# Kernel tuning notes

Measured on AMD Instinct MI355X. Metric: run time of the kernel, lower is better.

Reference implementation:

```python
import jax, jax.numpy as jnp
import numpy as np

APERTURE = 128
LN_EPS = 1e-6

def _layer_norm(y, g, b):
    mu = jnp.mean(y, axis=-1, keepdims=True)
    var = jnp.var(y, axis=-1, keepdims=True)
    return (y - mu) / jnp.sqrt(var + LN_EPS) * g + b

def setup_inputs() -> dict:
    key = jax.random.key(0)
    ks = jax.random.split(key, 12)
    B, S, D = 4, 4096, 1024
    gain = np.sqrt(2.0)
    xav = lambda k, fan_out, fan_in: jax.random.uniform(
        k, (fan_out, fan_in), jnp.float32,
        -gain * np.sqrt(6.0 / (fan_in + fan_out)), gain * np.sqrt(6.0 / (fan_in + fan_out)))
    return {
        "x": jax.random.normal(ks[0], (B, S, D), jnp.float32),
        "Wq": xav(ks[1], D, D),
        "Wk": xav(ks[2], D, D),
        "Wv": xav(ks[3], D, D),
        "Wo": xav(ks[4], D, D),
        "k1_w": xav(ks[5], D, D),
        "k1_b": jnp.full((D,), 0.1, jnp.float32),
        "k2_w": xav(ks[6], 1, D),
        "k2_b": jnp.full((1,), 0.1, jnp.float32),
        "ln_g": jnp.ones((D,), jnp.float32),
        "ln_b": jnp.zeros((D,), jnp.float32),
    }

def reference(x, Wq, Wk, Wv, Wo, k1_w, k1_b, k2_w, k2_b, ln_g, ln_b):
    B, S, D = x.shape
    scale = jnp.float32(1.0 / np.sqrt(D))
    neg_inf = jnp.float32(-np.inf)

    Q = x @ Wq.T  # [B,S,D]
    K = x @ Wk.T
    V = x @ Wv.T

    e = jnp.einsum('bsd,btd->bst', Q, K) * scale  # [B,S,S]

    # ignore_self: -inf on the diagonal
    i = jnp.arange(S)[:, None]
    j = jnp.arange(S)[None, :]
    e = jnp.where(i == j, neg_inf, e)

    # banded aperture mask: tril(e, ap) * triu(e, -ap); zeros of the product -> -inf
    d = j - i
    scope = jnp.where(d <= APERTURE, e, 0.0) * jnp.where(d >= -APERTURE, e, 0.0)
    e = jnp.where(scope == 0.0, neg_inf, e)

    alpha = jax.nn.softmax(e, axis=2)
    c = jnp.einsum('bst,btd->bsd', alpha, V)
    c = c @ Wo.T

    y = c + x
    y = _layer_norm(y, ln_g, ln_b)
    y = jax.nn.relu(y @ k1_w.T + k1_b)
    y = _layer_norm(y, ln_g, ln_b)
    y = jax.nn.sigmoid(y @ k2_w.T + k2_b)  # [B,S,1]
    return y.reshape(B, S)
```

## Files before the change

kernel.cpp:

```cpp
#include <hip/hip_runtime.h>
#include <math.h>

#define DD 1024
#define SS 4096
#define AP 128
#define LN_EPS 1e-6f
#define BK 32
#define BAND 384

typedef __bf16 bf16;
typedef __attribute__((ext_vector_type(4))) __bf16 bf16x4;
typedef __attribute__((ext_vector_type(8))) __bf16 bf16x8;
typedef __attribute__((ext_vector_type(4))) float f32x4;

#define GLOAD_LDS16(g, l)                                                   \
    __builtin_amdgcn_global_load_lds(                                        \
        (const __attribute__((address_space(1))) void*)(g),                  \
        (__attribute__((address_space(3))) void*)(l), 16, 0, 0)

__global__ __launch_bounds__(256) void prep_all(const float* __restrict__ x,
                                                const float* __restrict__ Wq,
                                                const float* __restrict__ Wk,
                                                const float* __restrict__ Wv,
                                                const float* __restrict__ Wo,
                                                const float* __restrict__ k1w,
                                                const float* __restrict__ k1b,
                                                const float* __restrict__ lng,
                                                const float* __restrict__ lnb,
                                                bf16* __restrict__ xb,
                                                bf16* __restrict__ Wob,
                                                bf16* __restrict__ k1g,
                                                bf16* __restrict__ Wtb,
                                                float* __restrict__ u1,
                                                float* __restrict__ c1b) {
    __shared__ float tile[64][65];
    const int bid = blockIdx.x;
    const int tid = threadIdx.x;
    if (bid < 16384) {
        const int i = (bid * 256 + tid) * 4;
        const float4 a = *(const float4*)(x + i);
        bf16x4 o;
        o[0] = (__bf16)a.x; o[1] = (__bf16)a.y; o[2] = (__bf16)a.z; o[3] = (__bf16)a.w;
        *(bf16x4*)(xb + i) = o;
        return;
    }
    if (bid < 18432) {
        const int b2 = bid - 16384;
        const int sel = b2 >> 10;
        const int bb = b2 & 1023;
        const float* s = sel ? k1w : Wo;
        bf16* d = sel ? k1g : Wob;
        const int i = (bb * 256 + tid) * 4;
        float4 a = *(const float4*)(s + i);
        if (sel) {
            const float4 g4 = *(const float4*)(lng + (i & (DD - 1)));
            a.x *= g4.x; a.y *= g4.y; a.z *= g4.z; a.w *= g4.w;
        }
        bf16x4 o;
        o[0] = (__bf16)a.x; o[1] = (__bf16)a.y; o[2] = (__bf16)a.z; o[3] = (__bf16)a.w;
        *(bf16x4*)(d + i) = o;
        return;
    }
    if (bid < 19200) {
        const int t = bid - 18432;
        const int tz = t >> 8;
        const int tb_ = t & 255;
        const float* in = (tz == 0) ? Wq : (tz == 1) ? Wk : Wv;
        bf16* out = Wtb + ((size_t)tz << 20);
        const int r0 = (tb_ >> 4) * 64, c0 = (tb_ & 15) * 64;
        const int lr = tid >> 4;
        const int lc = (tid & 15) * 4;
#pragma unroll
        for (int rr = 0; rr < 4; rr++) {
            const int row = lr + rr * 16;
            const float4 v = *(const float4*)(in + (size_t)(r0 + row) * DD + c0 + lc);
            tile[row][lc] = v.x; tile[row][lc + 1] = v.y;
            tile[row][lc + 2] = v.z; tile[row][lc + 3] = v.w;
        }
        __syncthreads();
#pragma unroll
        for (int rr = 0; rr < 4; rr++) {
            const int row = lr + rr * 16;
            bf16x4 o;
            o[0] = (__bf16)tile[lc + 0][row];
            o[1] = (__bf16)tile[lc + 1][row];
            o[2] = (__bf16)tile[lc + 2][row];
            o[3] = (__bf16)tile[lc + 3][row];
            *(bf16x4*)(out + (size_t)(c0 + row) * DD + r0 + lc) = o;
        }
        return;
    }
    const int pv = bid - 19200;
    const int lane = tid & 63, wave = tid >> 6;
    const int n = pv * 4 + wave;
    const float* row = k1w + (size_t)n * DD + lane * 16;
    float su = 0.f, sb = 0.f;
#pragma unroll
    for (int q = 0; q < 4; q++) {
        const float4 a = *(const float4*)(row + q * 4);
        const float4 g4 = *(const float4*)(lng + lane * 16 + q * 4);
        const float4 b4 = *(const float4*)(lnb + lane * 16 + q * 4);
        su += a.x * g4.x + a.y * g4.y + a.z * g4.z + a.w * g4.w;
        sb += a.x * b4.x + a.y * b4.y + a.z * b4.z + a.w * b4.w;
    }
#pragma unroll
    for (int off = 32; off > 0; off >>= 1) {
        su += __shfl_xor(su, off);
        sb += __shfl_xor(sb, off);
    }
    if (lane == 0) {
        u1[n] = su;
        c1b[n] = sb + k1b[n];
    }
}

__global__ __launch_bounds__(256) void gemm_pair(const bf16* __restrict__ A0,
                                                 const bf16* __restrict__ W0,
                                                 bf16* __restrict__ O0,
                                                 const bf16* __restrict__ A1,
                                                 const bf16* __restrict__ W1,
                                                 bf16* __restrict__ O1) {
    const bf16* A = blockIdx.z ? A1 : A0;
    const bf16* W = blockIdx.z ? W1 : W0;
    bf16* O = blockIdx.z ? O1 : O0;
    __shared__ bf16 As[128 * BK];
    __shared__ bf16 Bs[128 * BK];
    const int tid = threadIdx.x;
    const int lane = tid & 63;
    const int wave = tid >> 6;
    const int wm = wave & 1;
    const int wn = wave >> 1;
    const int m0 = blockIdx.y * 128;
    const int n0 = blockIdx.x * 128;

    const int c = wave * 64 + lane;
    const int ar = c >> 2;
    const int ac = (c & 3) << 3;
    char* AsB = (char*)As;
    char* BsB = (char*)Bs;
    const int lr = lane & 15;
    const int lk = (lane >> 4) << 3;

    f32x4 acc[4][4] = {};

    for (int kt = 0; kt < DD; kt += BK) {
        const bf16* ga0 = A + (size_t)(m0 + ar) * DD + kt + ac;
        const bf16* gb0 = W + (size_t)(n0 + ar) * DD + kt + ac;
        GLOAD_LDS16(ga0, AsB + wave * 1024);
        GLOAD_LDS16(ga0 + (size_t)64 * DD, AsB + 4096 + wave * 1024);
        GLOAD_LDS16(gb0, BsB + wave * 1024);
        GLOAD_LDS16(gb0 + (size_t)64 * DD, BsB + 4096 + wave * 1024);
        __syncthreads();

        bf16x8 af[4], bfr[4];
#pragma unroll
        for (int i = 0; i < 4; i++)
            af[i] = *(const bf16x8*)&As[(wm * 64 + i * 16 + lr) * BK + lk];
#pragma unroll
        for (int j = 0; j < 4; j++)
            bfr[j] = *(const bf16x8*)&Bs[(wn * 64 + j * 16 + lr) * BK + lk];
#pragma unroll
        for (int i = 0; i < 4; i++)
#pragma unroll
            for (int j = 0; j < 4; j++)
                acc[i][j] = __builtin_amdgcn_mfma_f32_16x16x32_bf16(af[i], bfr[j], acc[i][j], 0, 0, 0);
        __syncthreads();
    }

#pragma unroll
    for (int i = 0; i < 4; i++) {
        const int row = m0 + wm * 64 + i * 16 + ((lane >> 4) << 2);
#pragma unroll
        for (int j = 0; j < 4; j++) {
            const int col = n0 + wn * 64 + j * 16 + (lane & 15);
#pragma unroll
            for (int rr = 0; rr < 4; rr++)
                O[(size_t)(row + rr) * DD + col] = (__bf16)acc[i][j][rr];
        }
    }
}


#define KL_STAGE_A(tt, hh, bb)                                               \
    {                                                                        \
        const bf16* gp_ = Aop + gofsA + (tt) * 64 + (hh) * 32;               \
        GLOAD_LDS16(gp_, smem + (bb) + (hh) * 16384 + ldsW);                 \
        GLOAD_LDS16(gp_ + (size_t)128 * DD,                                  \
                    smem + (bb) + (hh) * 16384 + 8192 + ldsW);               \
    }
#define KL_STAGE_B(tt, hh, bb)                                               \
    {                                                                        \
        const bf16* gp_ = Bop + gofsB + (tt) * 64 + (hh) * 32;               \
        GLOAD_LDS16(gp_, smem + (bb) + 32768 + (hh) * 16384 + ldsW);         \
        GLOAD_LDS16(gp_ + (size_t)128 * DD,                                  \
                    smem + (bb) + 32768 + (hh) * 16384 + 8192 + ldsW);       \
    }
#define KL_READS_A(ks, mh)                                                   \
    af[0] = *(const bf16x8*)(sA + bufo + (ks) * 16384 + (mh) * 4096);        \
    af[1] = *(const bf16x8*)(sA + bufo + (ks) * 16384 + (mh) * 4096 + 1024); \
    af[2] = *(const bf16x8*)(sA + bufo + (ks) * 16384 + (mh) * 4096 + 2048); \
    af[3] = *(const bf16x8*)(sA + bufo + (ks) * 16384 + (mh) * 4096 + 3072);
#define KL_READS_B(ks)                                                       \
    bfr[0] = *(const bf16x8*)(sB + bufo + (ks) * 16384);                     \
    bfr[1] = *(const bf16x8*)(sB + bufo + (ks) * 16384 + 1024);              \
    bfr[2] = *(const bf16x8*)(sB + bufo + (ks) * 16384 + 2048);              \
    bfr[3] = *(const bf16x8*)(sB + bufo + (ks) * 16384 + 3072);
#define KL_MFMA4(I, MH)                                                      \
    acc[(MH) * 4 + I][0] = __builtin_amdgcn_mfma_f32_16x16x32_bf16(af[I], bfr[0], acc[(MH) * 4 + I][0], 0, 0, 0); \
    acc[(MH) * 4 + I][1] = __builtin_amdgcn_mfma_f32_16x16x32_bf16(af[I], bfr[1], acc[(MH) * 4 + I][1], 0, 0, 0); \
    acc[(MH) * 4 + I][2] = __builtin_amdgcn_mfma_f32_16x16x32_bf16(af[I], bfr[2], acc[(MH) * 4 + I][2], 0, 0, 0); \
    acc[(MH) * 4 + I][3] = __builtin_amdgcn_mfma_f32_16x16x32_bf16(af[I], bfr[3], acc[(MH) * 4 + I][3], 0, 0, 0);
#define KL_MFMA16(MH)                                                        \
    __builtin_amdgcn_s_setprio(1);                                           \
    KL_MFMA4(0, MH) KL_MFMA4(1, MH) KL_MFMA4(2, MH) KL_MFMA4(3, MH)          \
    __builtin_amdgcn_s_setprio(0);
#define KL_BARRIER(N) asm volatile("s_waitcnt vmcnt(" #N ")\n\ts_barrier" ::: "memory")

__device__ __forceinline__ void kloop256(const bf16* __restrict__ Aop,
                                         const bf16* __restrict__ Bop,
                                         const int m0, const int n0,
                                         char* smem, f32x4 (&acc)[8][4],
                                         const int tid, const int lane,
                                         const int wave, const int wm, const int wn) {
    const int grow = tid >> 2;
    const int gslot = (tid & 3) ^ ((tid >> 3) & 3);
    const size_t gofsA = (size_t)(m0 + grow) * DD + gslot * 8;
    const size_t gofsB = (size_t)(n0 + grow) * DD + gslot * 8;
    const int ldsW = wave * 1024;
    const int sxo = (((lane >> 4) ^ ((lane >> 1) & 3)) << 4);
    const char* sA = smem + wm * 8192 + (lane & 15) * 64 + sxo;
    const char* sB = smem + 32768 + wn * 4096 + (lane & 15) * 64 + sxo;

    bf16x8 af[4], bfr[4];

    KL_STAGE_A(0, 0, 0) KL_STAGE_B(0, 0, 0)
    KL_STAGE_A(0, 1, 0) KL_STAGE_B(0, 1, 0)
    KL_STAGE_A(1, 0, 65536) KL_STAGE_B(1, 0, 65536)

    int bufo = 0;
    for (int t = 0; t < 15; t++) {
        const int nb = bufo ^ 65536;
        KL_BARRIER(8);
        KL_READS_A(0, 0) KL_READS_B(0)
        KL_STAGE_A(t + 1, 1, nb)
        KL_MFMA16(0)
        KL_READS_A(0, 1)
        KL_STAGE_B(t + 1, 1, nb)
        KL_MFMA16(1)
        KL_BARRIER(8);
        KL_READS_A(1, 0) KL_READS_B(1)
        if (t < 14) { KL_STAGE_A(t + 2, 0, bufo) }
        KL_MFMA16(0)
        KL_READS_A(1, 1)
        if (t < 14) { KL_STAGE_B(t + 2, 0, bufo) }
        KL_MFMA16(1)
        bufo = nb;
    }
    KL_BARRIER(4);
    KL_READS_A(0, 0) KL_READS_B(0)
    KL_MFMA16(0)
    KL_READS_A(0, 1)
    KL_MFMA16(1)
    KL_BARRIER(0);
    KL_READS_A(1, 0) KL_READS_B(1)
    KL_MFMA16(0)
    KL_READS_A(1, 1)
    KL_MFMA16(1)
}

__global__ __launch_bounds__(512) void gemm_uv(const bf16* __restrict__ xb,
                                               const bf16* __restrict__ Gt,
                                               const bf16* __restrict__ W2,
                                               bf16* __restrict__ Ub,
                                               bf16* __restrict__ Vt2) {
    __shared__ char smem[131072];
    const int s = blockIdx.x;
    const int half = s >> 8;
    const int sh = s & 255;
    const int p = (sh & 7) | ((sh >> 5) << 3);
    const int q = (sh >> 3) & 3;
    const bf16* A;
    const bf16* W;
    bf16* O;
    int m0, n0;
    size_t ldo;
    if (half == 0) {
        A = xb; W = Gt; O = Ub;
        m0 = p * 256; n0 = q * 256; ldo = DD;
    } else {
        A = W2; W = xb; O = Vt2;
        m0 = q * 256; n0 = p * 256; ldo = (size_t)4 * SS;
    }
    const int tid = threadIdx.x;
    const int lane = tid & 63;
    const int wave = tid >> 6;
    const int wm = wave & 1;
    const int wn = wave >> 1;

    f32x4 acc[8][4] = {};
    kloop256(A, W, m0, n0, smem, acc, tid, lane, wave, wm, wn);

#pragma unroll
    for (int a = 0; a < 8; a++) {
        const int row = m0 + wm * 128 + a * 16 + ((lane >> 4) << 2);
#pragma unroll
        for (int j = 0; j < 4; j++) {
            const int col = n0 + wn * 64 + j * 16 + (lane & 15);
#pragma unroll
            for (int rr = 0; rr < 4; rr++)
                O[(size_t)(row + rr) * ldo + col] = (__bf16)acc[a][j][rr];
        }
    }
}

__global__ __launch_bounds__(512) void gemm_k1(const bf16* __restrict__ T,
                                               const bf16* __restrict__ k1g,
                                               const float* __restrict__ part_t,
                                               const float* __restrict__ u1,
                                               const float* __restrict__ c1b,
                                               const float* __restrict__ lng,
                                               const float* __restrict__ k2w,
                                               float* __restrict__ part_h) {
    __shared__ char smem[131072];
    __shared__ float lmu[256], lrs[256];
    const int m0 = blockIdx.x * 256;
    const int n0 = blockIdx.y * 256;
    const int tid = threadIdx.x;
    const int lane = tid & 63;
    const int wave = tid >> 6;
    const int wm = wave & 1;
    const int wn = wave >> 1;

    if (tid < 256) {
        const float* p = part_t + (size_t)(m0 + tid) * 32;
        float s1 = 0.f, s2 = 0.f;
#pragma unroll
        for (int s = 0; s < 8; s++) {
            const float4 v = *(const float4*)(p + s * 4);
            s1 += v.x + v.z;
            s2 += v.y + v.w;
        }
        const float m = s1 * (1.f / DD);
        lmu[tid] = m;
        lrs[tid] = rsqrtf(s2 * (1.f / DD) - m * m + LN_EPS);
    }
    __syncthreads();

    f32x4 acc[8][4] = {};
    kloop256(T, k1g, m0, n0, smem, acc, tid, lane, wave, wm, wn);

    float u1v[4], cbv[4], ugv[4];
#pragma unroll
    for (int j = 0; j < 4; j++) {
        const int col = n0 + wn * 64 + j * 16 + (lane & 15);
        u1v[j] = u1[col];
        cbv[j] = c1b[col];
        ugv[j] = lng[col] * k2w[col];
    }
    const int strip = blockIdx.y * 4 + wn;
#pragma unroll
    for (int a = 0; a < 8; a++) {
#pragma unroll
        for (int rr = 0; rr < 4; rr++) {
            const int lrow = wm * 128 + a * 16 + ((lane >> 4) << 2) + rr;
            const int row = m0 + lrow;
            const float mr = lmu[lrow], rs = lrs[lrow];
            float s1 = 0.f, s2 = 0.f, s3 = 0.f;
#pragma unroll
            for (int j = 0; j < 4; j++) {
                const float v = rs * (acc[a][j][rr] - mr * u1v[j]) + cbv[j];
                const float h = fmaxf(v, 0.f);
                s1 += h; s2 += h * h; s3 += h * ugv[j];
            }
#pragma unroll
            for (int off = 8; off > 0; off >>= 1) {
                s1 += __shfl_xor(s1, off);
                s2 += __shfl_xor(s2, off);
                s3 += __shfl_xor(s3, off);
            }
            if ((lane & 15) == 0) {
                float* p = part_h + (size_t)row * 48 + strip * 3;
                p[0] = s1; p[1] = s2; p[2] = s3;
            }
        }
    }
}

__global__ __launch_bounds__(512) void attn_sp(const bf16* __restrict__ U,
                                               const bf16* __restrict__ X,
                                               bf16* __restrict__ P) {
    __shared__ bf16 As[64 * BK];
    __shared__ bf16 Bs[384 * BK];
    const int s = blockIdx.x;
    const int t = (s & 7) * 32 + ((s >> 3) >> 1) * 2 + ((s >> 3) & 1);
    const int tid = threadIdx.x;
    const int lane = tid & 63;
    const int wave = tid >> 6;
    const int wm = wave & 1;
    const int wn = wave >> 1;
    const int m0 = t * 64;
    const long w0 = (long)(t >> 1) * 128 - 128;

    const int grow = tid >> 2;
    const int gslot = (tid & 3) ^ ((tid >> 3) & 3);
    const size_t gofsA = (size_t)(m0 + (grow & 63)) * DD + gslot * 8;
    const long gofsB = (w0 + grow) * (long)DD + gslot * 8;
    const int ldsW = wave * 1024;
    const int sxo = (((lane >> 4) ^ ((lane >> 1) & 3)) << 4);
    const char* sA = (const char*)As + (lane & 15) * 64 + sxo;
    const char* sB = (const char*)Bs + (lane & 15) * 64 + sxo;

    f32x4 acc[2][6] = {};

    for (int kt = 0; kt < DD; kt += BK) {
        if (wave < 4) { GLOAD_LDS16(U + gofsA + kt, (char*)As + ldsW); }
        GLOAD_LDS16(X + gofsB + kt, (char*)Bs + ldsW);
        GLOAD_LDS16(X + gofsB + (long)128 * DD + kt, (char*)Bs + 8192 + ldsW);
        GLOAD_LDS16(X + gofsB + (long)256 * DD + kt, (char*)Bs + 16384 + ldsW);
        __syncthreads();

        bf16x8 af[2], bfr[6];
#pragma unroll
        for (int i = 0; i < 2; i++)
            af[i] = *(const bf16x8*)(sA + wm * 2048 + i * 1024);
#pragma unroll
        for (int j = 0; j < 6; j++)
            bfr[j] = *(const bf16x8*)(sB + wn * 6144 + j * 1024);
#pragma unroll
        for (int i = 0; i < 2; i++)
#pragma unroll
            for (int j = 0; j < 6; j++)
                acc[i][j] = __builtin_amdgcn_mfma_f32_16x16x32_bf16(af[i], bfr[j], acc[i][j], 0, 0, 0);
        __syncthreads();
    }

    float* lredm = (float*)As;
    float* lreds = lredm + 256;
    const int rbase = wm * 32 + ((lane >> 4) << 2);
    const int ib = (t << 6) & (SS - 1);
    const int jst = ((t >> 1) & 31) * 128 - 128;
    const float scale = 0.03125f;

    float pmx[2][4];
#pragma unroll
    for (int i = 0; i < 2; i++)
#pragma unroll
        for (int rr = 0; rr < 4; rr++) {
            const int irow = ib + rbase + i * 16 + rr;
            float mx = -INFINITY;
#pragma unroll
            for (int j = 0; j < 6; j++) {
                const int jg = jst + wn * 96 + j * 16 + (lane & 15);
                const int dj = jg - irow;
                const bool valid = (jg >= 0) && (jg < SS) && (dj != 0) && (dj <= AP) && (dj >= -AP);
                const float sv = valid ? acc[i][j][rr] * scale : -INFINITY;
                acc[i][j][rr] = sv;
                mx = fmaxf(mx, sv);
            }
#pragma unroll
            for (int off = 8; off > 0; off >>= 1) mx = fmaxf(mx, __shfl_xor(mx, off));
            pmx[i][rr] = mx;
        }
    if ((lane & 15) == 0) {
#pragma unroll
        for (int i = 0; i < 2; i++)
#pragma unroll
            for (int rr = 0; rr < 4; rr++)
                lredm[(rbase + i * 16 + rr) * 4 + wn] = pmx[i][rr];
    }
    __syncthreads();

    float lsum[2][4], mv[2][4];
#pragma unroll
    for (int i = 0; i < 2; i++)
#pragma unroll
        for (int rr = 0; rr < 4; rr++) {
            const int ri = (rbase + i * 16 + rr) * 4;
            mv[i][rr] = fmaxf(fmaxf(lredm[ri], lredm[ri + 1]),
                              fmaxf(lredm[ri + 2], lredm[ri + 3]));
            float su = 0.f;
#pragma unroll
            for (int j = 0; j < 6; j++) {
                const float e = __expf(acc[i][j][rr] - mv[i][rr]);
                acc[i][j][rr] = e;
                su += e;
            }
#pragma unroll
            for (int off = 8; off > 0; off >>= 1) su += __shfl_xor(su, off);
            lsum[i][rr] = su;
        }
    if ((lane & 15) == 0) {
#pragma unroll
        for (int i = 0; i < 2; i++)
#pragma unroll
            for (int rr = 0; rr < 4; rr++)
                lreds[(rbase + i * 16 + rr) * 4 + wn] = lsum[i][rr];
    }
    __syncthreads();

#pragma unroll
    for (int i = 0; i < 2; i++)
#pragma unroll
        for (int rr = 0; rr < 4; rr++) {
            const int ri = (rbase + i * 16 + rr) * 4;
            const float inv = 1.f / (lreds[ri] + lreds[ri + 1] + lreds[ri + 2] + lreds[ri + 3]);
            const size_t ro = (size_t)(m0 + rbase + i * 16 + rr) * BAND;
#pragma unroll
            for (int j = 0; j < 6; j++)
                P[ro + wn * 96 + j * 16 + (lane & 15)] = (__bf16)(acc[i][j][rr] * inv);
        }
}

__global__ __launch_bounds__(512) void attn_pv_mfma(const bf16* __restrict__ P,
                                                    const bf16* __restrict__ Vt,
                                                    const bf16* __restrict__ xres,
                                                    bf16* __restrict__ T,
                                                    float* __restrict__ part_t) {
    __shared__ bf16 As[128 * BK];
    __shared__ bf16 Bs[256 * BK];
    const int tid = threadIdx.x;
    const int lane = tid & 63;
    const int wave = tid >> 6;
    const int wm = wave & 1;
    const int wn = wave >> 1;
    const int t = blockIdx.x;
    const int m0 = t * 128;
    const int n0 = blockIdx.y * 256;
    const bf16* Wb = Vt + (long)t * 128 - 128;

    const int ar = tid >> 2;
    const int ac = (tid & 3) << 3;
    char* AsB = (char*)As;
    char* BsB = (char*)Bs;
    const int lr = lane & 15;
    const int lk = (lane >> 4) << 3;

    f32x4 acc[4][4] = {};

    for (int kt = 0; kt < BAND; kt += BK) {
        const bf16* ga0 = P + (size_t)(m0 + ar) * BAND + kt + ac;
        const bf16* gb0 = Wb + (size_t)(n0 + ar) * (4 * SS) + kt + ac;
        GLOAD_LDS16(ga0, AsB + wave * 1024);
        GLOAD_LDS16(gb0, BsB + wave * 1024);
        GLOAD_LDS16(gb0 + (size_t)128 * (4 * SS), BsB + 8192 + wave * 1024);
        __syncthreads();

        bf16x8 af[4], bfr[4];
#pragma unroll
        for (int i = 0; i < 4; i++)
            af[i] = *(const bf16x8*)&As[(wm * 64 + i * 16 + lr) * BK + lk];
#pragma unroll
        for (int j = 0; j < 4; j++)
            bfr[j] = *(const bf16x8*)&Bs[(wn * 64 + j * 16 + lr) * BK + lk];
#pragma unroll
        for (int i = 0; i < 4; i++)
#pragma unroll
            for (int j = 0; j < 4; j++)
                acc[i][j] = __builtin_amdgcn_mfma_f32_16x16x32_bf16(af[i], bfr[j], acc[i][j], 0, 0, 0);
        __syncthreads();
    }

    const int strip = blockIdx.y * 4 + wn;
#pragma unroll
    for (int i = 0; i < 4; i++) {
#pragma unroll
        for (int rr = 0; rr < 4; rr++) {
            const int row = m0 + wm * 64 + i * 16 + ((lane >> 4) << 2) + rr;
            float s1 = 0.f, s2 = 0.f;
#pragma unroll
            for (int j = 0; j < 4; j++) {
                const int col = n0 + wn * 64 + j * 16 + (lane & 15);
                const size_t idx = (size_t)row * DD + col;
                const __bf16 tv_b = (__bf16)(acc[i][j][rr] + (float)xres[idx]);
                T[idx] = tv_b;
                const float tv = (float)tv_b;
                s1 += tv; s2 += tv * tv;
            }
#pragma unroll
            for (int off = 8; off > 0; off >>= 1) {
                s1 += __shfl_xor(s1, off);
                s2 += __shfl_xor(s2, off);
            }
            if ((lane & 15) == 0) {
                float2 st; st.x = s1; st.y = s2;
                *(float2*)(part_t + (size_t)row * 32 + strip * 2) = st;
            }
        }
    }
}

__global__ __launch_bounds__(256) void ln_k2_p(const float* __restrict__ part_h,
                                               const float* __restrict__ g,
                                               const float* __restrict__ bta,
                                               const float* __restrict__ w2,
                                               const float* __restrict__ b2,
                                               float* __restrict__ out) {
    __shared__ float red[256], red2[256];
    const int tid = threadIdx.x;
    const float4 g4 = *(const float4*)(g + tid * 4);
    const float4 w4 = *(const float4*)(w2 + tid * 4);
    const float4 b4 = *(const float4*)(bta + tid * 4);
    red[tid] = g4.x * w4.x + g4.y * w4.y + g4.z * w4.z + g4.w * w4.w;
    red2[tid] = b4.x * w4.x + b4.y * w4.y + b4.z * w4.z + b4.w * w4.w;
    __syncthreads();
    for (int s = 128; s > 0; s >>= 1) {
        if (tid < s) { red[tid] += red[tid + s]; red2[tid] += red2[tid + s]; }
        __syncthreads();
    }
    const float sum_u = red[0];
    const float sum_bw = red2[0];

    const int r = blockIdx.x * 256 + tid;
    const float* p = part_h + (size_t)r * 48;
    float s1 = 0.f, s2 = 0.f, s3 = 0.f;
#pragma unroll
    for (int s = 0; s < 16; s++) {
        s1 += p[s * 3 + 0];
        s2 += p[s * 3 + 1];
        s3 += p[s * 3 + 2];
    }
    const float m = s1 * (1.f / DD);
    const float var = s2 * (1.f / DD) - m * m;
    const float rs = rsqrtf(var + LN_EPS);
    const float z = rs * (s3 - m * sum_u) + sum_bw + b2[0];
    out[r] = 1.f / (1.f + __expf(-z));
}

extern "C" void kernel_launch(void* const* d_in, const int* in_sizes, int n_in,
                              void* d_out, int out_size, void* d_ws, size_t ws_size,
                              hipStream_t stream) {
    const float* x   = (const float*)d_in[0];
    const float* Wq  = (const float*)d_in[1];
    const float* Wk  = (const float*)d_in[2];
    const float* Wv  = (const float*)d_in[3];
    const float* Wo  = (const float*)d_in[4];
    const float* k1w = (const float*)d_in[5];
    const float* k1b = (const float*)d_in[6];
    const float* k2w = (const float*)d_in[7];
    const float* k2b = (const float*)d_in[8];
    const float* lng = (const float*)d_in[9];
    const float* lnb = (const float*)d_in[10];
    float* out = (float*)d_out;

    const int N = 4 * SS;
    char* ws = (char*)d_ws;
    bf16*  Ub   = (bf16*)(ws);
    bf16*  xb   = (bf16*)(ws + ((size_t)32  << 20));
    bf16*  Vt2  = (bf16*)(ws + ((size_t)64  << 20));
    bf16*  P    = (bf16*)(ws + ((size_t)96  << 20));
    bf16*  T    = (bf16*)(ws + ((size_t)164 << 20));
    bf16*  Wtb  = (bf16*)(ws + ((size_t)196 << 20));
    bf16*  Wqtb = Wtb;
    bf16*  Wktb = Wqtb + (1 << 20);
    bf16*  Wvtb = Wktb + (1 << 20);
    bf16*  Wob  = Wvtb + (1 << 20);
    bf16*  k1g  = Wob  + (1 << 20);
    bf16*  Gtb  = k1g  + (1 << 20);
    bf16*  W2b  = Gtb  + (1 << 20);
    float* u1     = (float*)(ws + ((size_t)210 << 20));
    float* c1b    = u1 + DD;
    float* part_t = (float*)(ws + ((size_t)211 << 20));
    float* part_h = (float*)(ws + ((size_t)214 << 20));

    dim3 tb(256);

    prep_all<<<19456, tb, 0, stream>>>(x, Wq, Wk, Wv, Wo, k1w, k1b, lng, lnb,
                                       xb, Wob, k1g, Wtb, u1, c1b);

    gemm_pair<<<dim3(8, 8, 2), tb, 0, stream>>>(Wktb, Wqtb, Gtb, Wob, Wvtb, W2b);

    gemm_uv<<<512, dim3(512), 0, stream>>>(xb, Gtb, W2b, Ub, Vt2);

    attn_sp<<<256, dim3(512), 0, stream>>>(Ub, xb, P);
    attn_pv_mfma<<<dim3(N / 128, 4), dim3(512), 0, stream>>>(P, Vt2, xb, T, part_t);

    gemm_k1<<<dim3(64, 4), dim3(512), 0, stream>>>(T, k1g, part_t, u1, c1b, lng, k2w, part_h);
    ln_k2_p<<<N / 256, tb, 0, stream>>>(part_h, lng, lnb, k2w, k2b, out);
}
```

Baseline: 335.6 us.

## Double-buffer attn_sp band GEMM with async LDS loads and BK=64 stages

New measurement: 320.5 us, median of 2. 1.05x faster.

```diff
diff --git a/kernel.cpp b/kernel.cpp
--- a/kernel.cpp
+++ b/kernel.cpp
@@ -386,13 +386,40 @@
     }
 }
 
+#define SP_STAGE(tt, bb)                                                      \
+    {                                                                         \
+        const int kt_ = (tt) * 64;                                            \
+        GLOAD_LDS16(U + gofsA + kt_, smem + (bb) + ldsWA);                    \
+        GLOAD_LDS16(X + gofsB + kt_, smem + (bb) + 8192 + ldsW);              \
+        GLOAD_LDS16(X + gofsB + (long)128 * DD + kt_, smem + (bb) + 16384 + ldsW); \
+        GLOAD_LDS16(X + gofsB + (long)256 * DD + kt_, smem + (bb) + 24576 + ldsW); \
+        GLOAD_LDS16(X + gofsB + kt_ + 32, smem + (bb) + 32768 + ldsW);        \
+        GLOAD_LDS16(X + gofsB + (long)128 * DD + kt_ + 32, smem + (bb) + 40960 + ldsW); \
+        GLOAD_LDS16(X + gofsB + (long)256 * DD + kt_ + 32, smem + (bb) + 49152 + ldsW); \
+    }
+#define SP_READS(bb)                                                          \
+    _Pragma("unroll") for (int i_ = 0; i_ < 2; i_++) {                        \
+        a0[i_] = *(const bf16x8*)(sA + (bb) + wm * 2048 + i_ * 1024);         \
+        a1[i_] = *(const bf16x8*)(sA + (bb) + 4096 + wm * 2048 + i_ * 1024);  \
+    }                                                                         \
+    _Pragma("unroll") for (int j_ = 0; j_ < 6; j_++) {                        \
+        b0[j_] = *(const bf16x8*)(sB + (bb) + wn * 6144 + j_ * 1024);         \
+        b1[j_] = *(const bf16x8*)(sB + (bb) + 24576 + wn * 6144 + j_ * 1024); \
+    }
+#define SP_MFMA(AR, BR)                                                       \
+    __builtin_amdgcn_s_setprio(1);                                            \
+    _Pragma("unroll") for (int i_ = 0; i_ < 2; i_++)                          \
+        _Pragma("unroll") for (int j_ = 0; j_ < 6; j_++)                      \
+            acc[i_][j_] = __builtin_amdgcn_mfma_f32_16x16x32_bf16(AR[i_], BR[j_], acc[i_][j_], 0, 0, 0); \
+    __builtin_amdgcn_s_setprio(0);
+#define SP_LGBAR asm volatile("s_waitcnt lgkmcnt(0)\n\ts_barrier" ::: "memory")
+
 __global__ __launch_bounds__(512) void attn_sp(const bf16* __restrict__ U,
                                                const bf16* __restrict__ X,
                                                bf16* __restrict__ P) {
-    __shared__ bf16 As[64 * BK];
-    __shared__ bf16 Bs[384 * BK];
+    __shared__ char smem[114688];
     const int s = blockIdx.x;
-    const int t = (s & 7) * 32 + ((s >> 3) >> 1) * 2 + ((s >> 3) & 1);
+    const int t = (s & 7) * 32 + (s >> 3);
     const int tid = threadIdx.x;
     const int lane = tid & 63;
     const int wave = tid >> 6;
@@ -403,38 +430,41 @@
 
     const int grow = tid >> 2;
     const int gslot = (tid & 3) ^ ((tid >> 3) & 3);
-    const size_t gofsA = (size_t)(m0 + (grow & 63)) * DD + gslot * 8;
+    const size_t gofsA = (size_t)(m0 + (grow & 63)) * DD + gslot * 8 + (wave >> 2) * 32;
     const long gofsB = (w0 + grow) * (long)DD + gslot * 8;
+    const int ldsWA = (wave & 3) * 1024 + (wave >> 2) * 4096;
     const int ldsW = wave * 1024;
     const int sxo = (((lane >> 4) ^ ((lane >> 1) & 3)) << 4);
-    const char* sA = (const char*)As + (lane & 15) * 64 + sxo;
-    const char* sB = (const char*)Bs + (lane & 15) * 64 + sxo;
+    const char* sA = smem + (lane & 15) * 64 + sxo;
+    const char* sB = smem + 8192 + (lane & 15) * 64 + sxo;
 
     f32x4 acc[2][6] = {};
-
-    for (int kt = 0; kt < DD; kt += BK) {
-        if (wave < 4) { GLOAD_LDS16(U + gofsA + kt, (char*)As + ldsW); }
-        GLOAD_LDS16(X + gofsB + kt, (char*)Bs + ldsW);
-        GLOAD_LDS16(X + gofsB + (long)128 * DD + kt, (char*)Bs + 8192 + ldsW);
-        GLOAD_LDS16(X + gofsB + (long)256 * DD + kt, (char*)Bs + 16384 + ldsW);
-        __syncthreads();
-
-        bf16x8 af[2], bfr[6];
-#pragma unroll
-        for (int i = 0; i < 2; i++)
-            af[i] = *(const bf16x8*)(sA + wm * 2048 + i * 1024);
-#pragma unroll
-        for (int j = 0; j < 6; j++)
-            bfr[j] = *(const bf16x8*)(sB + wn * 6144 + j * 1024);
-#pragma unroll
-        for (int i = 0; i < 2; i++)
-#pragma unroll
-            for (int j = 0; j < 6; j++)
-                acc[i][j] = __builtin_amdgcn_mfma_f32_16x16x32_bf16(af[i], bfr[j], acc[i][j], 0, 0, 0);
-        __syncthreads();
-    }
-
-    float* lredm = (float*)As;
+    bf16x8 a0[2], b0[6], a1[2], b1[6];
+
+    SP_STAGE(0, 0)
+    SP_STAGE(1, 57344)
+
+#pragma unroll 1
+    for (int tt = 0; tt < 14; tt++) {
+        const int bb = (tt & 1) * 57344;
+        KL_BARRIER(7);
+        SP_READS(bb)
+        SP_MFMA(a0, b0)
+        SP_LGBAR;
+        SP_STAGE(tt + 2, bb)
+        SP_MFMA(a1, b1)
+    }
+    KL_BARRIER(7);
+    SP_READS(0)
+    SP_MFMA(a0, b0)
+    SP_MFMA(a1, b1)
+    KL_BARRIER(0);
+    SP_READS(57344)
+    SP_MFMA(a0, b0)
+    SP_MFMA(a1, b1)
+    __syncthreads();
+
+    float* lredm = (float*)smem;
     float* lreds = lredm + 256;
     const int rbase = wm * 32 + ((lane >> 4) << 2);
     const int ib = (t << 6) & (SS - 1);
```
